# Kernel optimization log

Measured on AMD Instinct MI355X. Metric: run time of the kernel, lower is better.

Reference implementation:

```python
import jax, jax.numpy as jnp
import numpy as np

HEAD_DIM = 128
NUM_HEADS = 16
NUM_KV_HEADS = 8
HIDDEN = 2048
SEQ = 4096
BATCH = 1
ROPE_THETA = 1e6
RMS_EPS = 1e-6


def rms_norm(x, w, eps=RMS_EPS):
    # normalize over the last (head_dim) axis
    var = jnp.mean(jnp.square(x), axis=-1, keepdims=True)
    return x * jax.lax.rsqrt(var + eps) * w


def apply_rope(x, positions):
    # x: [B, S, H, D], positions: [B, S]; rotate-half (GPT-NeoX style)
    d = x.shape[-1]
    inv_freq = 1.0 / (ROPE_THETA ** (jnp.arange(0, d, 2, dtype=jnp.float32) / d))  # [D/2]
    ang = positions.astype(jnp.float32)[..., None] * inv_freq  # [B, S, D/2]
    cos = jnp.cos(ang)[:, :, None, :]  # [B, S, 1, D/2]
    sin = jnp.sin(ang)[:, :, None, :]
    x1, x2 = x[..., : d // 2], x[..., d // 2 :]
    return jnp.concatenate([x1 * cos - x2 * sin, x2 * cos + x1 * sin], axis=-1)


def setup_inputs() -> dict:
    key = jax.random.key(0)
    ks = jax.random.split(key, 8)
    s = 0.02
    return {
        "positions": jnp.broadcast_to(jnp.arange(SEQ, dtype=jnp.int64 if jax.config.jax_enable_x64 else jnp.int32)[None, :], (BATCH, SEQ)),
        "hidden_states": jax.random.normal(ks[0], (BATCH, SEQ, HIDDEN), jnp.float32),
        "wq": jax.random.normal(ks[1], (NUM_HEADS * HEAD_DIM, HIDDEN), jnp.float32) * s,
        "bq": jnp.zeros((NUM_HEADS * HEAD_DIM,), jnp.float32),
        "wk": jax.random.normal(ks[2], (NUM_KV_HEADS * HEAD_DIM, HIDDEN), jnp.float32) * s,
        "bk": jnp.zeros((NUM_KV_HEADS * HEAD_DIM,), jnp.float32),
        "wv": jax.random.normal(ks[3], (NUM_KV_HEADS * HEAD_DIM, HIDDEN), jnp.float32) * s,
        "bv": jnp.zeros((NUM_KV_HEADS * HEAD_DIM,), jnp.float32),
        "wo": jax.random.normal(ks[4], (HIDDEN, NUM_HEADS * HEAD_DIM), jnp.float32) * s,
        "bo": jnp.zeros((HIDDEN,), jnp.float32),
        "q_norm_w": jnp.ones((HEAD_DIM,), jnp.float32),
        "k_norm_w": jnp.ones((HEAD_DIM,), jnp.float32),
    }


def reference(positions, hidden_states, wq, bq, wk, bk, wv, bv, wo, bo, q_norm_w, k_norm_w):
    B, S, _ = hidden_states.shape
    H, Hkv, D = NUM_HEADS, NUM_KV_HEADS, HEAD_DIM
    scaling = D ** -0.5

    q = (hidden_states @ wq.T + bq).reshape(B, S, H, D)
    k = (hidden_states @ wk.T + bk).reshape(B, S, Hkv, D)
    v = (hidden_states @ wv.T + bv).reshape(B, S, Hkv, D)

    q = apply_rope(rms_norm(q, q_norm_w), positions)
    k = apply_rope(rms_norm(k, k_norm_w), positions)

    # GQA: repeat_interleave kv heads to match query heads
    rep = H // Hkv
    k = jnp.repeat(k, rep, axis=2)  # [B, S, H, D]
    v = jnp.repeat(v, rep, axis=2)

    # scores: [B, H, S, S]
    scores = jnp.einsum("bqhd,bkhd->bhqk", q, k) * scaling
    causal = jnp.tril(jnp.ones((S, S), dtype=bool))
    scores = jnp.where(causal[None, None], scores, -jnp.inf)
    attn = jax.nn.softmax(scores, axis=-1)

    out = jnp.einsum("bhqk,bkhd->bqhd", attn, v).reshape(B, S, H * D)
    return out @ wo.T + bo
```

## Files before the change

### kernel.cpp

```cpp
#include <hip/hip_runtime.h>
#include <hip/hip_bf16.h>

#define SQ   4096
#define HIDN 2048
#define NH   16
#define NKV  8
#define HD   128
#define QD   2048
#define KD   1024
#define KVB  64

typedef __bf16 bf16x8 __attribute__((ext_vector_type(8)));
typedef float  f32x4  __attribute__((ext_vector_type(4)));

__device__ __forceinline__ float b2f(unsigned short u) {
    union { float f; unsigned int i; } v; v.i = ((unsigned int)u) << 16; return v.f;
}
__device__ __forceinline__ unsigned short f2b(float f) {
    union { float f; unsigned int i; } v; v.f = f;
    unsigned int i = v.i;
    return (unsigned short)((i + 0x7FFFu + ((i >> 16) & 1u)) >> 16);
}

__device__ __forceinline__ void gload_lds16(const void* g, void* l) {
    __builtin_amdgcn_global_load_lds(
        (const __attribute__((address_space(1))) unsigned int*)g,
        (__attribute__((address_space(3))) unsigned int*)l, 16, 0, 0);
}

#define MFMA16(a, b, c) __builtin_amdgcn_mfma_f32_16x16x32_bf16(a, b, c, 0, 0, 0)

#define DPP_ROR(x, n) __int_as_float(__builtin_amdgcn_update_dpp(            \
    __float_as_int(x), __float_as_int(x), 0x120 + (n), 0xF, 0xF, false))

__device__ __forceinline__ float rowmax16(float x) {
    x = fmaxf(x, DPP_ROR(x, 1));
    x = fmaxf(x, DPP_ROR(x, 2));
    x = fmaxf(x, DPP_ROR(x, 4));
    x = fmaxf(x, DPP_ROR(x, 8));
    return x;
}
__device__ __forceinline__ float rowsum16(float x) {
    x += DPP_ROR(x, 1);
    x += DPP_ROR(x, 2);
    x += DPP_ROR(x, 4);
    x += DPP_ROR(x, 8);
    return x;
}

__global__ __launch_bounds__(256) void cvt_all(const float* __restrict__ h,
                                               const float* __restrict__ wq,
                                               const float* __restrict__ wk,
                                               const float* __restrict__ wv,
                                               const float* __restrict__ wo,
                                               unsigned short* __restrict__ oh,
                                               unsigned short* __restrict__ owq,
                                               unsigned short* __restrict__ owk,
                                               unsigned short* __restrict__ owv,
                                               unsigned short* __restrict__ owo) {
    int i = blockIdx.x * 256 + threadIdx.x;
    const float* src; unsigned short* dst; int off;
    if (i < 2097152)      { src = h;  dst = oh;  off = i; }
    else if (i < 3145728) { src = wq; dst = owq; off = i - 2097152; }
    else if (i < 3670016) { src = wk; dst = owk; off = i - 3145728; }
    else if (i < 4194304) { src = wv; dst = owv; off = i - 3670016; }
    else                  { src = wo; dst = owo; off = i - 4194304; }
    float4 v = ((const float4*)src)[off];
    ushort4 u;
    u.x = f2b(v.x); u.y = f2b(v.y); u.z = f2b(v.z); u.w = f2b(v.w);
    ((ushort4*)dst)[off] = u;
}

__global__ __launch_bounds__(256) void rope_table(const int* __restrict__ pos,
                                                  float* __restrict__ cosT,
                                                  float* __restrict__ sinT) {
    int i = blockIdx.x * 256 + threadIdx.x;
    int s = i >> 6, j = i & 63;
    float invf = __expf(-(float)j * (1.3815510557964274f / 6.4f));
    float a = (float)pos[s] * invf;
    cosT[i] = cosf(a);
    sinT[i] = sinf(a);
}

__global__ __launch_bounds__(256) void gemm_qkv(const unsigned short* __restrict__ A,
                                                const unsigned short* __restrict__ B,
                                                const float* __restrict__ bq,
                                                const float* __restrict__ bk,
                                                const float* __restrict__ bv,
                                                unsigned short* __restrict__ qp,
                                                unsigned short* __restrict__ kp,
                                                unsigned short* __restrict__ vtp) {
    const int M = 4096, K = 2048;
    __shared__ unsigned short As[128 * 32];
    __shared__ unsigned short Bs[128 * 32];
    const int tid = threadIdx.x, wid = tid >> 6, lane = tid & 63;
    const int g = lane >> 4, c = lane & 15;
    const int wr = wid >> 1, wc = wid & 1;
    const int orig = blockIdx.y * gridDim.x + blockIdx.x;
    const int cpx = (gridDim.x * gridDim.y) >> 3;
    const int wg = (orig & 7) * cpx + (orig >> 3);
    const int bx = wg % gridDim.x, by = wg / gridDim.x;
    const long rowbase = (long)by * 128;
    const long colbase = (long)bx * 128;

    f32x4 acc[4][4];
#pragma unroll
    for (int m = 0; m < 4; ++m)
#pragma unroll
        for (int n = 0; n < 4; ++n) acc[m][n] = (f32x4){0.f, 0.f, 0.f, 0.f};

    const int ch0 = (wid * 2) * 64 + lane;
    const int ch1 = (wid * 2 + 1) * 64 + lane;

    for (int kt = 0; kt < K; kt += 32) {
        gload_lds16(A + ((rowbase + (ch0 >> 2)) * K + kt + (ch0 & 3) * 8),
                    As + (wid * 2) * 64 * 8);
        gload_lds16(B + ((colbase + (ch0 >> 2)) * K + kt + (ch0 & 3) * 8),
                    Bs + (wid * 2) * 64 * 8);
        gload_lds16(A + ((rowbase + (ch1 >> 2)) * K + kt + (ch1 & 3) * 8),
                    As + (wid * 2 + 1) * 64 * 8);
        gload_lds16(B + ((colbase + (ch1 >> 2)) * K + kt + (ch1 & 3) * 8),
                    Bs + (wid * 2 + 1) * 64 * 8);
        __syncthreads();
        bf16x8 a[4], b[4];
#pragma unroll
        for (int m = 0; m < 4; ++m)
            a[m] = *(const bf16x8*)(As + (wr * 64 + m * 16 + c) * 32 + g * 8);
#pragma unroll
        for (int n = 0; n < 4; ++n)
            b[n] = *(const bf16x8*)(Bs + (wc * 64 + n * 16 + c) * 32 + g * 8);
#pragma unroll
        for (int m = 0; m < 4; ++m)
#pragma unroll
            for (int n = 0; n < 4; ++n) acc[m][n] = MFMA16(a[m], b[n], acc[m][n]);
        __syncthreads();
    }

#pragma unroll
    for (int m = 0; m < 4; ++m) {
        const long grow0 = rowbase + wr * 64 + m * 16 + g * 4;
#pragma unroll
        for (int n = 0; n < 4; ++n) {
            const long gcol = colbase + wc * 64 + n * 16 + c;
            if (colbase < 2048) {
                const float bs = bq[gcol];
#pragma unroll
                for (int r = 0; r < 4; ++r)
                    qp[(grow0 + r) * QD + gcol] = f2b(acc[m][n][r] + bs);
            } else if (colbase < 3072) {
                const float bs = bk[gcol - 2048];
#pragma unroll
                for (int r = 0; r < 4; ++r)
                    kp[(grow0 + r) * KD + (gcol - 2048)] = f2b(acc[m][n][r] + bs);
            } else {
                const float bs = bv[gcol - 3072];
                ushort4 pk;
                pk.x = f2b(acc[m][n][0] + bs);
                pk.y = f2b(acc[m][n][1] + bs);
                pk.z = f2b(acc[m][n][2] + bs);
                pk.w = f2b(acc[m][n][3] + bs);
                *(ushort4*)(vtp + (gcol - 3072) * (long)M + grow0) = pk;
            }
        }
    }
}

__global__ __launch_bounds__(256) void gemm_o(const unsigned short* __restrict__ A,
                                              const unsigned short* __restrict__ B,
                                              const float* __restrict__ bias,
                                              float* __restrict__ Cout,
                                              int M, int N, int K) {
    __shared__ unsigned short As[128 * 32];
    __shared__ unsigned short Bs[128 * 32];
    const int tid = threadIdx.x, wid = tid >> 6, lane = tid & 63;
    const int g = lane >> 4, c = lane & 15;
    const int wr = wid >> 1, wc = wid & 1;
    const int orig = blockIdx.y * gridDim.x + blockIdx.x;
    const int cpx = (gridDim.x * gridDim.y) >> 3;
    const int wg = (orig & 7) * cpx + (orig >> 3);
    const int bx = wg % gridDim.x, by = wg / gridDim.x;
    const long rowbase = (long)by * 128;
    const long colbase = (long)bx * 128;

    f32x4 acc[4][4];
#pragma unroll
    for (int m = 0; m < 4; ++m)
#pragma unroll
        for (int n = 0; n < 4; ++n) acc[m][n] = (f32x4){0.f, 0.f, 0.f, 0.f};

    const int ch0 = (wid * 2) * 64 + lane;
    const int ch1 = (wid * 2 + 1) * 64 + lane;

    for (int kt = 0; kt < K; kt += 32) {
        gload_lds16(A + ((rowbase + (ch0 >> 2)) * K + kt + (ch0 & 3) * 8),
                    As + (wid * 2) * 64 * 8);
        gload_lds16(B + ((colbase + (ch0 >> 2)) * K + kt + (ch0 & 3) * 8),
                    Bs + (wid * 2) * 64 * 8);
        gload_lds16(A + ((rowbase + (ch1 >> 2)) * K + kt + (ch1 & 3) * 8),
                    As + (wid * 2 + 1) * 64 * 8);
        gload_lds16(B + ((colbase + (ch1 >> 2)) * K + kt + (ch1 & 3) * 8),
                    Bs + (wid * 2 + 1) * 64 * 8);
        __syncthreads();
        bf16x8 a[4], b[4];
#pragma unroll
        for (int m = 0; m < 4; ++m)
            a[m] = *(const bf16x8*)(As + (wr * 64 + m * 16 + c) * 32 + g * 8);
#pragma unroll
        for (int n = 0; n < 4; ++n)
            b[n] = *(const bf16x8*)(Bs + (wc * 64 + n * 16 + c) * 32 + g * 8);
#pragma unroll
        for (int m = 0; m < 4; ++m)
#pragma unroll
            for (int n = 0; n < 4; ++n) acc[m][n] = MFMA16(a[m], b[n], acc[m][n]);
        __syncthreads();
    }

#pragma unroll
    for (int m = 0; m < 4; ++m) {
        const long grow0 = rowbase + wr * 64 + m * 16 + g * 4;
#pragma unroll
        for (int n = 0; n < 4; ++n) {
            const long gcol = colbase + wc * 64 + n * 16 + c;
            const float bs = bias[gcol];
#pragma unroll
            for (int r = 0; r < 4; ++r)
                Cout[(grow0 + r) * N + gcol] = acc[m][n][r] + bs;
        }
    }
}

__global__ __launch_bounds__(256) void norm_rope(const unsigned short* __restrict__ proj,
                                                 int nh,
                                                 const float* __restrict__ w,
                                                 const float* __restrict__ cosT,
                                                 const float* __restrict__ sinT,
                                                 unsigned short* __restrict__ outt,
                                                 float oscale) {
    int wv = (blockIdx.x * 256 + threadIdx.x) >> 6;
    int lane = threadIdx.x & 63;
    int s = wv / nh, h = wv - s * nh;
    const unsigned short* p = proj + (size_t)s * (nh * HD) + h * HD;
    float x1 = b2f(p[lane]);
    float x2 = b2f(p[lane + 64]);
    float ss = x1 * x1 + x2 * x2;
#pragma unroll
    for (int d = 1; d < 64; d <<= 1) ss += __shfl_xor(ss, d);
    float r = rsqrtf(ss * (1.f / 128.f) + 1e-6f);
    x1 *= r * w[lane];
    x2 *= r * w[lane + 64];
    float cs = cosT[s * 64 + lane], sn = sinT[s * 64 + lane];
    unsigned short o1 = f2b((x1 * cs - x2 * sn) * oscale);
    unsigned short o2 = f2b((x2 * cs + x1 * sn) * oscale);
    unsigned short* q = outt + ((size_t)h * SQ + s) * HD;
    q[lane] = o1;
    q[lane + 64] = o2;
}

__global__ __launch_bounds__(256, 2) void fattn(const unsigned short* __restrict__ qt,
                                                const unsigned short* __restrict__ kt,
                                                const unsigned short* __restrict__ vt,
                                                unsigned short* __restrict__ aout) {
    __shared__ unsigned short Ks[2][KVB * HD];
    __shared__ unsigned short Vs[2][HD * KVB];
    const int tid = threadIdx.x, wid = tid >> 6, lane = tid & 63;
    const int g = lane >> 4, c = lane & 15;
    const int id = blockIdx.x;
    const int qb = (id < 256) ? (31 - (id >> 4)) : ((id - 256) >> 4);
    const int h = id & 15, hk = h >> 1;
    const int row0 = qb * 128 + wid * 32;
    const unsigned short* qh = qt + (size_t)h * SQ * HD;
    const unsigned short* kh = kt + (size_t)hk * SQ * HD;
    const unsigned short* vh = vt + (size_t)hk * HD * SQ;
    const int ntile = 2 * qb + 2;

    bf16x8 qa[2][4];
#pragma unroll
    for (int ks = 0; ks < 4; ++ks) {
        qa[0][ks] = *(const bf16x8*)(qh + (size_t)(row0 + c) * HD + ks * 32 + g * 8);
        qa[1][ks] = *(const bf16x8*)(qh + (size_t)(row0 + 16 + c) * HD + ks * 32 + g * 8);
    }

    f32x4 o[2][8];
#pragma unroll
    for (int m = 0; m < 2; ++m)
#pragma unroll
        for (int df = 0; df < 8; ++df) o[m][df] = (f32x4){0.f, 0.f, 0.f, 0.f};
    float mrow[2][4], lrow[2][4];
#pragma unroll
    for (int m = 0; m < 2; ++m)
#pragma unroll
        for (int r = 0; r < 4; ++r) { mrow[m][r] = -1e30f; lrow[m][r] = 0.f; }

    auto stage = [&](int b, int t) {
        const int kv0 = t * KVB;
#pragma unroll
        for (int i = 0; i < 4; ++i) {
            const int gi = wid * 4 + i;
            const int P = gi * 1024 + lane * 16;
            const int rk = P >> 8;
            const int Uk = (P & 255) ^ (((rk >> 2) & 7) << 4);
            gload_lds16(kh + (size_t)(kv0 + rk) * HD + (Uk >> 1),
                        (char*)Ks[b] + gi * 1024);
            const int rv = P >> 7;
            const int Uv = (P & 127) ^ ((rv & 7) << 4);
            gload_lds16(vh + (size_t)rv * SQ + kv0 + (Uv >> 1),
                        (char*)Vs[b] + gi * 1024);
        }
    };

    stage(0, 0);
    asm volatile("s_waitcnt vmcnt(0)" ::: "memory");
    __syncthreads();

    int bcur = 0;
    for (int j = 0; j < ntile; ++j) {
        const int kv0 = j * KVB;
        if (j + 1 < ntile) stage(bcur ^ 1, j + 1);

        f32x4 sa[2][4];
#pragma unroll
        for (int m = 0; m < 2; ++m)
#pragma unroll
            for (int nf = 0; nf < 4; ++nf) sa[m][nf] = (f32x4){0.f, 0.f, 0.f, 0.f};
        __builtin_amdgcn_s_setprio(1);
#pragma unroll
        for (int nf = 0; nf < 4; ++nf) {
            const int krow = (c << 2) + nf;
            const int key = (c & 7) << 4;
#pragma unroll
            for (int ks = 0; ks < 4; ++ks) {
                bf16x8 kf = *(const bf16x8*)((const char*)Ks[bcur] + krow * 256 +
                                             ((ks * 64 + g * 16) ^ key));
                sa[0][nf] = MFMA16(qa[0][ks], kf, sa[0][nf]);
                sa[1][nf] = MFMA16(qa[1][ks], kf, sa[1][nf]);
            }
        }
        __builtin_amdgcn_s_setprio(0);
        asm volatile("s_waitcnt lgkmcnt(0)" ::: "memory");
        __builtin_amdgcn_s_barrier();
        char* plw = (char*)Ks[bcur] + wid * 4096;

        if (kv0 + 63 > row0) {
#pragma unroll
            for (int m = 0; m < 2; ++m) {
                const int rb = row0 + m * 16;
#pragma unroll
                for (int nf = 0; nf < 4; ++nf) {
                    const int col = kv0 + (c << 2) + nf;
#pragma unroll
                    for (int r = 0; r < 4; ++r) {
                        int row = rb + g * 4 + r;
                        if (col > row) sa[m][nf][r] = -1e30f;
                    }
                }
            }
        }
        float nmax[2][4];
        int small = 1;
#pragma unroll
        for (int m = 0; m < 2; ++m)
#pragma unroll
            for (int r = 0; r < 4; ++r) {
                float mx = fmaxf(fmaxf(sa[m][0][r], sa[m][1][r]),
                                 fmaxf(sa[m][2][r], sa[m][3][r]));
                mx = rowmax16(mx);
                nmax[m][r] = mx;
                small &= (mx <= mrow[m][r] + 8.0f);
            }
        if (!__all(small)) {
#pragma unroll
            for (int m = 0; m < 2; ++m) {
                float psc[4];
#pragma unroll
                for (int r = 0; r < 4; ++r) {
                    float mn = fmaxf(mrow[m][r], nmax[m][r]);
                    psc[r] = __builtin_amdgcn_exp2f(mrow[m][r] - mn);
                    mrow[m][r] = mn;
                    lrow[m][r] *= psc[r];
                }
#pragma unroll
                for (int df = 0; df < 8; ++df)
#pragma unroll
                    for (int r = 0; r < 4; ++r) o[m][df][r] *= psc[r];
            }
        }
#pragma unroll
        for (int m = 0; m < 2; ++m)
#pragma unroll
            for (int r = 0; r < 4; ++r) {
                float rs = 0.f;
#pragma unroll
                for (int nf = 0; nf < 4; ++nf) {
                    float p = __builtin_amdgcn_exp2f(sa[m][nf][r] - mrow[m][r]);
                    sa[m][nf][r] = p;
                    rs += p;
                }
                lrow[m][r] += rowsum16(rs);
            }
#pragma unroll
        for (int m = 0; m < 2; ++m)
#pragma unroll
            for (int r = 0; r < 4; ++r) {
                unsigned int lo, hi;
                asm("v_cvt_pk_bf16_f32 %0, %1, %2"
                    : "=v"(lo) : "v"(sa[m][0][r]), "v"(sa[m][1][r]));
                asm("v_cvt_pk_bf16_f32 %0, %1, %2"
                    : "=v"(hi) : "v"(sa[m][2][r]), "v"(sa[m][3][r]));
                const int row = m * 16 + g * 4 + r;
                const int pcol = (c * 8) ^ ((row & 7) << 4);
                *(uint2*)(plw + row * 128 + pcol) = make_uint2(lo, hi);
            }
        asm volatile("s_waitcnt lgkmcnt(0)" ::: "memory");
        __builtin_amdgcn_s_setprio(1);
#pragma unroll
        for (int ks = 0; ks < 2; ++ks) {
            const int pk_ = (ks * 64 + g * 16) ^ ((c & 7) << 4);
            bf16x8 pa0 = *(const bf16x8*)(plw + c * 128 + pk_);
            bf16x8 pa1 = *(const bf16x8*)(plw + (16 + c) * 128 + pk_);
#pragma unroll
            for (int df = 0; df < 8; ++df) {
                const int rd = df * 16 + c;
                bf16x8 vb = *(const bf16x8*)((const char*)Vs[bcur] + rd * 128 +
                                             ((ks * 64 + g * 16) ^ ((rd & 7) << 4)));
                o[0][df] = MFMA16(pa0, vb, o[0][df]);
                o[1][df] = MFMA16(pa1, vb, o[1][df]);
            }
        }
        __builtin_amdgcn_s_setprio(0);

        asm volatile("s_waitcnt vmcnt(0)" ::: "memory");
        __syncthreads();
        bcur ^= 1;
    }

#pragma unroll
    for (int m = 0; m < 2; ++m) {
        const int rb = row0 + m * 16;
        float inv[4];
#pragma unroll
        for (int r = 0; r < 4; ++r) inv[r] = 1.f / lrow[m][r];
#pragma unroll
        for (int df = 0; df < 8; ++df)
#pragma unroll
            for (int r = 0; r < 4; ++r) {
                size_t row = rb + g * 4 + r;
                aout[row * QD + h * HD + df * 16 + c] = f2b(o[m][df][r] * inv[r]);
            }
    }
}

extern "C" void kernel_launch(void* const* d_in, const int* in_sizes, int n_in,
                              void* d_out, int out_size, void* d_ws, size_t ws_size,
                              hipStream_t stream) {
    const int*   positions = (const int*)d_in[0];
    const float* hidden    = (const float*)d_in[1];
    const float* wq        = (const float*)d_in[2];
    const float* bq        = (const float*)d_in[3];
    const float* wk        = (const float*)d_in[4];
    const float* bk        = (const float*)d_in[5];
    const float* wv        = (const float*)d_in[6];
    const float* bv        = (const float*)d_in[7];
    const float* wo        = (const float*)d_in[8];
    const float* bo        = (const float*)d_in[9];
    const float* qnw       = (const float*)d_in[10];
    const float* knw       = (const float*)d_in[11];
    float* out = (float*)d_out;

    char* w = (char*)d_ws;
    unsigned short* hidden_b = (unsigned short*)(w);
    unsigned short* wqkv_b   = (unsigned short*)(w + 16777216);
    unsigned short* wq_b     = (unsigned short*)(w + 16777216);
    unsigned short* wk_b     = (unsigned short*)(w + 25165824);
    unsigned short* wv_b     = (unsigned short*)(w + 29360128);
    unsigned short* wo_b     = (unsigned short*)(w + 33554432);
    unsigned short* qproj    = (unsigned short*)(w + 41943040);
    unsigned short* kproj    = (unsigned short*)(w + 58720256);
    unsigned short* q_t      = (unsigned short*)(w + 67108864);
    unsigned short* k_t      = (unsigned short*)(w + 83886080);
    unsigned short* v_t      = (unsigned short*)(w + 92274688);
    float*          cosT     = (float*)(w + 100663296);
    float*          sinT     = (float*)(w + 101711872);
    unsigned short* attn     = qproj;

    cvt_all<<<20480, 256, 0, stream>>>(hidden, wq, wk, wv, wo,
                                       hidden_b, wq_b, wk_b, wv_b, wo_b);
    rope_table<<<SQ * 64 / 256, 256, 0, stream>>>(positions, cosT, sinT);
    gemm_qkv<<<dim3(32, 32), 256, 0, stream>>>(hidden_b, wqkv_b, bq, bk, bv,
                                               qproj, kproj, v_t);
    norm_rope<<<SQ * NH / 4, 256, 0, stream>>>(qproj, NH, qnw, cosT, sinT, q_t,
                                               (float)(0.08838834764831845 * 1.4426950408889634));
    norm_rope<<<SQ * NKV / 4, 256, 0, stream>>>(kproj, NKV, knw, cosT, sinT, k_t, 1.0f);
    fattn<<<512, 256, 0, stream>>>(q_t, k_t, v_t, attn);
    gemm_o<<<dim3(QD / 128, SQ / 128), 256, 0, stream>>>(attn, wo_b, bo, out, SQ, QD, HIDN);
}
```

Measured before the change: 474.5 us.

## Split causal attention KV range across segments with a separate combine kernel

Splits each 128-row query block's KV tile range into 1 to 4 segments depending on its length, raising the grid from 512 to 1280 blocks. Each block writes unnormalized bf16 partial outputs plus per-row max and sum, and a new fcombine kernel merges them. Warps whose rows lie entirely above the current KV tile now skip the MFMA and softmax work for that tile. The goal is better load balance and occupancy across CUs, at the cost of an extra kernel launch, partial-result global traffic, and precision loss from storing partial outputs in bf16. Workspace regions such as hidden_b, kproj and cosT are reused for the partials, which is only safe because they are dead by then.

```diff
diff --git a/kernel.cpp b/kernel.cpp
--- a/kernel.cpp
+++ b/kernel.cpp
@@ -259,19 +259,27 @@
 __global__ __launch_bounds__(256, 2) void fattn(const unsigned short* __restrict__ qt,
                                                 const unsigned short* __restrict__ kt,
                                                 const unsigned short* __restrict__ vt,
-                                                unsigned short* __restrict__ aout) {
+                                                unsigned short* __restrict__ pw0,
+                                                unsigned short* __restrict__ pw1,
+                                                float2* __restrict__ mlb) {
     __shared__ unsigned short Ks[2][KVB * HD];
     __shared__ unsigned short Vs[2][HD * KVB];
     const int tid = threadIdx.x, wid = tid >> 6, lane = tid & 63;
     const int g = lane >> 4, c = lane & 15;
     const int id = blockIdx.x;
-    const int qb = (id < 256) ? (31 - (id >> 4)) : ((id - 256) >> 4);
-    const int h = id & 15, hk = h >> 1;
+    const int h = id & 15, sr = id >> 4, s = 79 - sr;
+    int qb, seg, nseg;
+    if (s < 8)       { qb = s;                    nseg = 1; seg = 0; }
+    else if (s < 24) { qb = 8 + ((s - 8) >> 1);   nseg = 2; seg = (s - 8) & 1; }
+    else if (s < 48) { qb = 16 + (s - 24) / 3;    nseg = 3; seg = (s - 24) % 3; }
+    else             { qb = 24 + ((s - 48) >> 2); nseg = 4; seg = (s - 48) & 3; }
+    const int T = 2 * qb + 2;
+    const int t0 = seg * T / nseg, t1 = (seg + 1) * T / nseg;
+    const int hk = h >> 1;
     const int row0 = qb * 128 + wid * 32;
     const unsigned short* qh = qt + (size_t)h * SQ * HD;
     const unsigned short* kh = kt + (size_t)hk * SQ * HD;
     const unsigned short* vh = vt + (size_t)hk * HD * SQ;
-    const int ntile = 2 * qb + 2;
 
     bf16x8 qa[2][4];
 #pragma unroll
@@ -308,145 +316,195 @@
         }
     };
 
-    stage(0, 0);
+    stage(0, t0);
     asm volatile("s_waitcnt vmcnt(0)" ::: "memory");
     __syncthreads();
 
     int bcur = 0;
-    for (int j = 0; j < ntile; ++j) {
+    for (int j = t0; j < t1; ++j) {
         const int kv0 = j * KVB;
-        if (j + 1 < ntile) stage(bcur ^ 1, j + 1);
-
+        if (j + 1 < t1) stage(bcur ^ 1, j + 1);
+
+        const bool act = (kv0 <= row0 + 31);
         f32x4 sa[2][4];
 #pragma unroll
         for (int m = 0; m < 2; ++m)
 #pragma unroll
             for (int nf = 0; nf < 4; ++nf) sa[m][nf] = (f32x4){0.f, 0.f, 0.f, 0.f};
-        __builtin_amdgcn_s_setprio(1);
-#pragma unroll
-        for (int nf = 0; nf < 4; ++nf) {
-            const int krow = (c << 2) + nf;
-            const int key = (c & 7) << 4;
-#pragma unroll
-            for (int ks = 0; ks < 4; ++ks) {
-                bf16x8 kf = *(const bf16x8*)((const char*)Ks[bcur] + krow * 256 +
-                                             ((ks * 64 + g * 16) ^ key));
-                sa[0][nf] = MFMA16(qa[0][ks], kf, sa[0][nf]);
-                sa[1][nf] = MFMA16(qa[1][ks], kf, sa[1][nf]);
-            }
+        if (act) {
+            __builtin_amdgcn_s_setprio(1);
+#pragma unroll
+            for (int nf = 0; nf < 4; ++nf) {
+                const int krow = (c << 2) + nf;
+                const int key = (c & 7) << 4;
+#pragma unroll
+                for (int ks = 0; ks < 4; ++ks) {
+                    bf16x8 kf = *(const bf16x8*)((const char*)Ks[bcur] + krow * 256 +
+                                                 ((ks * 64 + g * 16) ^ key));
+                    sa[0][nf] = MFMA16(qa[0][ks], kf, sa[0][nf]);
+                    sa[1][nf] = MFMA16(qa[1][ks], kf, sa[1][nf]);
+                }
+            }
+            __builtin_amdgcn_s_setprio(0);
         }
-        __builtin_amdgcn_s_setprio(0);
         asm volatile("s_waitcnt lgkmcnt(0)" ::: "memory");
         __builtin_amdgcn_s_barrier();
         char* plw = (char*)Ks[bcur] + wid * 4096;
 
-        if (kv0 + 63 > row0) {
-#pragma unroll
-            for (int m = 0; m < 2; ++m) {
-                const int rb = row0 + m * 16;
-#pragma unroll
-                for (int nf = 0; nf < 4; ++nf) {
-                    const int col = kv0 + (c << 2) + nf;
+        if (act) {
+            if (kv0 + 63 > row0) {
+#pragma unroll
+                for (int m = 0; m < 2; ++m) {
+                    const int rb = row0 + m * 16;
+#pragma unroll
+                    for (int nf = 0; nf < 4; ++nf) {
+                        const int col = kv0 + (c << 2) + nf;
+#pragma unroll
+                        for (int r = 0; r < 4; ++r) {
+                            int row = rb + g * 4 + r;
+                            if (col > row) sa[m][nf][r] = -1e30f;
+                        }
+                    }
+                }
+            }
+            float nmax[2][4];
+            int small = 1;
+#pragma unroll
+            for (int m = 0; m < 2; ++m)
+#pragma unroll
+                for (int r = 0; r < 4; ++r) {
+                    float mx = fmaxf(fmaxf(sa[m][0][r], sa[m][1][r]),
+                                     fmaxf(sa[m][2][r], sa[m][3][r]));
+                    mx = rowmax16(mx);
+                    nmax[m][r] = mx;
+                    small &= (mx <= mrow[m][r] + 8.0f);
+                }
+            if (!__all(small)) {
+#pragma unroll
+                for (int m = 0; m < 2; ++m) {
+                    float psc[4];
 #pragma unroll
                     for (int r = 0; r < 4; ++r) {
-                        int row = rb + g * 4 + r;
-                        if (col > row) sa[m][nf][r] = -1e30f;
+                        float mn = fmaxf(mrow[m][r], nmax[m][r]);
+                        psc[r] = __builtin_amdgcn_exp2f(mrow[m][r] - mn);
+                        mrow[m][r] = mn;
+                        lrow[m][r] *= psc[r];
                     }
-                }
-            }
+#pragma unroll
+                    for (int df = 0; df < 8; ++df)
+#pragma unroll
+                        for (int r = 0; r < 4; ++r) o[m][df][r] *= psc[r];
+                }
+            }
+#pragma unroll
+            for (int m = 0; m < 2; ++m)
+#pragma unroll
+                for (int r = 0; r < 4; ++r) {
+                    float rs = 0.f;
+#pragma unroll
+                    for (int nf = 0; nf < 4; ++nf) {
+                        float p = __builtin_amdgcn_exp2f(sa[m][nf][r] - mrow[m][r]);
+                        sa[m][nf][r] = p;
+                        rs += p;
+                    }
+                    lrow[m][r] += rowsum16(rs);
+                }
+#pragma unroll
+            for (int m = 0; m < 2; ++m)
+#pragma unroll
+                for (int r = 0; r < 4; ++r) {
+                    unsigned int lo, hi;
+                    asm("v_cvt_pk_bf16_f32 %0, %1, %2"
+                        : "=v"(lo) : "v"(sa[m][0][r]), "v"(sa[m][1][r]));
+                    asm("v_cvt_pk_bf16_f32 %0, %1, %2"
+                        : "=v"(hi) : "v"(sa[m][2][r]), "v"(sa[m][3][r]));
+                    const int row = m * 16 + g * 4 + r;
+                    const int pcol = (c * 8) ^ ((row & 7) << 4);
+                    *(uint2*)(plw + row * 128 + pcol) = make_uint2(lo, hi);
+                }
+            asm volatile("s_waitcnt lgkmcnt(0)" ::: "memory");
+            __builtin_amdgcn_s_setprio(1);
+#pragma unroll
+            for (int ks = 0; ks < 2; ++ks) {
+                const int pk_ = (ks * 64 + g * 16) ^ ((c & 7) << 4);
+                bf16x8 pa0 = *(const bf16x8*)(plw + c * 128 + pk_);
+                bf16x8 pa1 = *(const bf16x8*)(plw + (16 + c) * 128 + pk_);
+#pragma unroll
+                for (int df = 0; df < 8; ++df) {
+                    const int rd = df * 16 + c;
+                    bf16x8 vb = *(const bf16x8*)((const char*)Vs[bcur] + rd * 128 +
+                                                 ((ks * 64 + g * 16) ^ ((rd & 7) << 4)));
+                    o[0][df] = MFMA16(pa0, vb, o[0][df]);
+                    o[1][df] = MFMA16(pa1, vb, o[1][df]);
+                }
+            }
+            __builtin_amdgcn_s_setprio(0);
         }
-        float nmax[2][4];
-        int small = 1;
-#pragma unroll
-        for (int m = 0; m < 2; ++m)
-#pragma unroll
-            for (int r = 0; r < 4; ++r) {
-                float mx = fmaxf(fmaxf(sa[m][0][r], sa[m][1][r]),
-                                 fmaxf(sa[m][2][r], sa[m][3][r]));
-                mx = rowmax16(mx);
-                nmax[m][r] = mx;
-                small &= (mx <= mrow[m][r] + 8.0f);
-            }
-        if (!__all(small)) {
-#pragma unroll
-            for (int m = 0; m < 2; ++m) {
-                float psc[4];
-#pragma unroll
-                for (int r = 0; r < 4; ++r) {
-                    float mn = fmaxf(mrow[m][r], nmax[m][r]);
-                    psc[r] = __builtin_amdgcn_exp2f(mrow[m][r] - mn);
-                    mrow[m][r] = mn;
-                    lrow[m][r] *= psc[r];
-                }
-#pragma unroll
-                for (int df = 0; df < 8; ++df)
-#pragma unroll
-                    for (int r = 0; r < 4; ++r) o[m][df][r] *= psc[r];
-            }
-        }
-#pragma unroll
-        for (int m = 0; m < 2; ++m)
-#pragma unroll
-            for (int r = 0; r < 4; ++r) {
-                float rs = 0.f;
-#pragma unroll
-                for (int nf = 0; nf < 4; ++nf) {
-                    float p = __builtin_amdgcn_exp2f(sa[m][nf][r] - mrow[m][r]);
-                    sa[m][nf][r] = p;
-                    rs += p;
-                }
-                lrow[m][r] += rowsum16(rs);
-            }
-#pragma unroll
-        for (int m = 0; m < 2; ++m)
-#pragma unroll
-            for (int r = 0; r < 4; ++r) {
-                unsigned int lo, hi;
-                asm("v_cvt_pk_bf16_f32 %0, %1, %2"
-                    : "=v"(lo) : "v"(sa[m][0][r]), "v"(sa[m][1][r]));
-                asm("v_cvt_pk_bf16_f32 %0, %1, %2"
-                    : "=v"(hi) : "v"(sa[m][2][r]), "v"(sa[m][3][r]));
-                const int row = m * 16 + g * 4 + r;
-                const int pcol = (c * 8) ^ ((row & 7) << 4);
-                *(uint2*)(plw + row * 128 + pcol) = make_uint2(lo, hi);
-            }
-        asm volatile("s_waitcnt lgkmcnt(0)" ::: "memory");
-        __builtin_amdgcn_s_setprio(1);
-#pragma unroll
-        for (int ks = 0; ks < 2; ++ks) {
-            const int pk_ = (ks * 64 + g * 16) ^ ((c & 7) << 4);
-            bf16x8 pa0 = *(const bf16x8*)(plw + c * 128 + pk_);
-            bf16x8 pa1 = *(const bf16x8*)(plw + (16 + c) * 128 + pk_);
-#pragma unroll
-            for (int df = 0; df < 8; ++df) {
-                const int rd = df * 16 + c;
-                bf16x8 vb = *(const bf16x8*)((const char*)Vs[bcur] + rd * 128 +
-                                             ((ks * 64 + g * 16) ^ ((rd & 7) << 4)));
-                o[0][df] = MFMA16(pa0, vb, o[0][df]);
-                o[1][df] = MFMA16(pa1, vb, o[1][df]);
-            }
-        }
-        __builtin_amdgcn_s_setprio(0);
 
         asm volatile("s_waitcnt vmcnt(0)" ::: "memory");
         __syncthreads();
         bcur ^= 1;
     }
 
-#pragma unroll
-    for (int m = 0; m < 2; ++m) {
-        const int rb = row0 + m * 16;
-        float inv[4];
-#pragma unroll
-        for (int r = 0; r < 4; ++r) inv[r] = 1.f / lrow[m][r];
+    unsigned short* op = (id < 1024) ? (pw0 + (size_t)id * 16384)
+                                     : (pw1 + (size_t)(id - 1024) * 16384);
+#pragma unroll
+    for (int m = 0; m < 2; ++m)
 #pragma unroll
         for (int df = 0; df < 8; ++df)
 #pragma unroll
             for (int r = 0; r < 4; ++r) {
-                size_t row = rb + g * 4 + r;
-                aout[row * QD + h * HD + df * 16 + c] = f2b(o[m][df][r] * inv[r]);
-            }
-    }
+                const int row = wid * 32 + m * 16 + g * 4 + r;
+                op[row * 128 + df * 16 + c] = f2b(o[m][df][r]);
+            }
+    if (c == 0) {
+#pragma unroll
+        for (int m = 0; m < 2; ++m)
+#pragma unroll
+            for (int r = 0; r < 4; ++r) {
+                const int row = wid * 32 + m * 16 + g * 4 + r;
+                mlb[(size_t)id * 128 + row] = make_float2(mrow[m][r], lrow[m][r]);
+            }
+    }
+}
+
+__global__ __launch_bounds__(256) void fcombine(const unsigned short* __restrict__ pw0,
+                                                const unsigned short* __restrict__ pw1,
+                                                const float2* __restrict__ mlb,
+                                                unsigned short* __restrict__ aout) {
+    const int gid = blockIdx.x * 8 + (threadIdx.x >> 5);
+    const int h = gid >> 12, row = gid & 4095;
+    const int qb = row >> 7, rloc = row & 127;
+    const int d0 = (threadIdx.x & 31) * 4;
+    int nseg, sbase;
+    if (qb < 8)       { nseg = 1; sbase = qb; }
+    else if (qb < 16) { nseg = 2; sbase = 8 + 2 * (qb - 8); }
+    else if (qb < 24) { nseg = 3; sbase = 24 + 3 * (qb - 16); }
+    else              { nseg = 4; sbase = 48 + 4 * (qb - 24); }
+    float M = -1e30f;
+    for (int k = 0; k < nseg; ++k) {
+        const int slot = (79 - (sbase + k)) * 16 + h;
+        M = fmaxf(M, mlb[(size_t)slot * 128 + rloc].x);
+    }
+    float L = 0.f, a0 = 0.f, a1 = 0.f, a2 = 0.f, a3 = 0.f;
+    for (int k = 0; k < nseg; ++k) {
+        const int slot = (79 - (sbase + k)) * 16 + h;
+        const float2 ml = mlb[(size_t)slot * 128 + rloc];
+        const float wgt = exp2f(ml.x - M);
+        L += wgt * ml.y;
+        const unsigned short* op = (slot < 1024) ? (pw0 + (size_t)slot * 16384)
+                                                 : (pw1 + (size_t)(slot - 1024) * 16384);
+        const ushort4 ov = *(const ushort4*)(op + rloc * 128 + d0);
+        a0 += wgt * b2f(ov.x);
+        a1 += wgt * b2f(ov.y);
+        a2 += wgt * b2f(ov.z);
+        a3 += wgt * b2f(ov.w);
+    }
+    const float inv = 1.f / L;
+    ushort4 r4;
+    r4.x = f2b(a0 * inv); r4.y = f2b(a1 * inv);
+    r4.z = f2b(a2 * inv); r4.w = f2b(a3 * inv);
+    *(ushort4*)(aout + (size_t)row * QD + h * HD + d0) = r4;
 }
 
 extern "C" void kernel_launch(void* const* d_in, const int* in_sizes, int n_in,
@@ -481,6 +539,9 @@
     float*          cosT     = (float*)(w + 100663296);
     float*          sinT     = (float*)(w + 101711872);
     unsigned short* attn     = qproj;
+    unsigned short* pw0      = (unsigned short*)(w);
+    unsigned short* pw1      = (unsigned short*)(w + 58720256);
+    float2*         mlb      = (float2*)(w + 100663296);
 
     cvt_all<<<20480, 256, 0, stream>>>(hidden, wq, wk, wv, wo,
                                        hidden_b, wq_b, wk_b, wv_b, wo_b);
@@ -490,6 +551,7 @@
     norm_rope<<<SQ * NH / 4, 256, 0, stream>>>(qproj, NH, qnw, cosT, sinT, q_t,
                                                (float)(0.08838834764831845 * 1.4426950408889634));
     norm_rope<<<SQ * NKV / 4, 256, 0, stream>>>(kproj, NKV, knw, cosT, sinT, k_t, 1.0f);
-    fattn<<<512, 256, 0, stream>>>(q_t, k_t, v_t, attn);
+    fattn<<<1280, 256, 0, stream>>>(q_t, k_t, v_t, pw0, pw1, mlb);
+    fcombine<<<8192, 256, 0, stream>>>(pw0, pw1, mlb, attn);
     gemm_o<<<dim3(QD / 128, SQ / 128), 256, 0, stream>>>(attn, wo_b, bo, out, SQ, QD, HIDN);
 }
```

After: 454.4 us. 4.2% less time.
